# Optimization experiments

Measured on AMD Instinct MI355X. Metric: run time of the kernel, lower is better.

## Reference

```python
import math
import jax, jax.numpy as jnp
import numpy as np

H = 12  # n_heads
NEG = -1e9

def setup_inputs() -> dict:
    key = jax.random.key(0)
    ks = jax.random.split(key, 5)
    B, S, D = 1, 4096, 768
    x = jax.random.normal(ks[0], (B, S, D), dtype=jnp.float32)
    Wqkv = jax.random.normal(ks[1], (D, 3 * D), dtype=jnp.float32) * (1.0 / math.sqrt(D))
    bqkv = jnp.zeros((3 * D,), dtype=jnp.float32)
    Wout = jax.random.normal(ks[2], (D, D), dtype=jnp.float32) * (1.0 / math.sqrt(D))
    bout = jnp.zeros((D,), dtype=jnp.float32)
    rel_bias = jax.random.normal(ks[3], (H, S, S), dtype=jnp.float32) * 0.02
    # additive causal mask: 0 on/below diagonal, large negative above
    causal_mask = jnp.where(jnp.tril(jnp.ones((S, S), dtype=bool)), 0.0, NEG).astype(jnp.float32)
    return {"x": x, "Wqkv": Wqkv, "bqkv": bqkv, "Wout": Wout, "bout": bout,
            "rel_bias": rel_bias, "causal_mask": causal_mask}

def reference(x, Wqkv, bqkv, Wout, bout, rel_bias, causal_mask):
    B, S, D = x.shape
    hd = D // H
    qkv = x @ Wqkv + bqkv                      # [B,S,3D]
    q, k, v = jnp.split(qkv, 3, axis=-1)
    def heads(t):  # [B,S,D] -> [B,H,S,hd]
        return t.reshape(B, S, H, hd).transpose(0, 2, 1, 3)
    q, k, v = heads(q), heads(k), heads(v)
    scores = jnp.einsum('bhqd,bhkd->bhqk', q, k) / math.sqrt(hd)
    scores = scores + rel_bias[None] + causal_mask[None, None]
    attn = jax.nn.softmax(scores, axis=-1)     # dropout p=0.0 -> identity
    out = jnp.einsum('bhqk,bhkd->bhqd', attn, v)
    out = out.transpose(0, 2, 1, 3).reshape(B, S, D)
    return out @ Wout + bout
```

## Files before the change

### kernel.cpp

```cpp
#include <hip/hip_runtime.h>
#include <stdint.h>

typedef _Float16 f16;
typedef _Float16 f16x8 __attribute__((ext_vector_type(8)));
typedef _Float16 f16x4 __attribute__((ext_vector_type(4)));
typedef float f32x4 __attribute__((ext_vector_type(4)));

#define NEGF -1e30f

static __device__ __forceinline__ f32x4 mfma16(f16x8 a, f16x8 b, f32x4 c) {
    return __builtin_amdgcn_mfma_f32_16x16x32_f16(a, b, c, 0, 0, 0);
}

static __device__ __forceinline__ void gload_lds16(const void* g, void* l) {
    __builtin_amdgcn_global_load_lds(
        (const __attribute__((address_space(1))) unsigned int*)g,
        (__attribute__((address_space(3))) unsigned int*)l, 16, 0, 0);
}

__global__ void cast_f32_f16(const float* __restrict__ src, f16* __restrict__ dst, int n) {
    int idx = blockIdx.x * blockDim.x + threadIdx.x;
    int stride = gridDim.x * blockDim.x;
    for (int i = idx * 4; i < n; i += stride * 4) {
        float4 v = *(const float4*)(src + i);
        f16x4 h;
        h[0] = (f16)v.x; h[1] = (f16)v.y; h[2] = (f16)v.z; h[3] = (f16)v.w;
        *(f16x4*)(dst + i) = h;
    }
}

__global__ void transpose_cast(const float* __restrict__ src, f16* __restrict__ dst, int R, int C) {
    __shared__ float tile[32][33];
    const int c0 = blockIdx.x * 32, r0 = blockIdx.y * 32;
    const int tx = threadIdx.x & 31, ty = threadIdx.x >> 5;
#pragma unroll
    for (int i = 0; i < 32; i += 8)
        tile[ty + i][tx] = src[(size_t)(r0 + ty + i) * C + c0 + tx];
    __syncthreads();
#pragma unroll
    for (int i = 0; i < 32; i += 8)
        dst[(size_t)(c0 + ty + i) * R + r0 + tx] = (f16)tile[tx][ty + i];
}

template <int MODE>
__global__ void __launch_bounds__(256, 2)
gemm_f16(const f16* __restrict__ A, const f16* __restrict__ Bt,
         const float* __restrict__ bias,
         f16* __restrict__ Qb, f16* __restrict__ Kb, f16* __restrict__ Vtb,
         float* __restrict__ Cout, int K, int N) {
    __shared__ alignas(16) f16 As[128 * 32];
    __shared__ alignas(16) f16 Bs[128 * 32];
    const int t = threadIdx.x;
    const int lane = t & 63, wid = t >> 6;
    const int wm = wid >> 1, wn = wid & 1;
    const int lr = lane & 15, lg = lane >> 4;
    const int m0 = blockIdx.y * 128, n0 = blockIdx.x * 128;
    f32x4 acc[4][4] = {};
    for (int k0 = 0; k0 < K; k0 += 32) {
#pragma unroll
        for (int i = 0; i < 2; i++) {
            const int cc = t + i * 256;
            const int rr = cc >> 2, ch = cc & 3;
            gload_lds16(A + (size_t)(m0 + rr) * K + k0 + ch * 8, (f16*)As + cc * 8);
            gload_lds16(Bt + (size_t)(n0 + rr) * K + k0 + ch * 8, (f16*)Bs + cc * 8);
        }
        __syncthreads();
        f16x8 af[4], bf[4];
#pragma unroll
        for (int i = 0; i < 4; i++)
            af[i] = *(const f16x8*)(As + (wm * 64 + i * 16 + lr) * 32 + lg * 8);
#pragma unroll
        for (int j = 0; j < 4; j++)
            bf[j] = *(const f16x8*)(Bs + (wn * 64 + j * 16 + lr) * 32 + lg * 8);
#pragma unroll
        for (int i = 0; i < 4; i++)
#pragma unroll
            for (int j = 0; j < 4; j++)
                acc[i][j] = mfma16(af[i], bf[j], acc[i][j]);
        __syncthreads();
    }
#pragma unroll
    for (int i = 0; i < 4; i++) {
#pragma unroll
        for (int j = 0; j < 4; j++) {
            const int n_g = n0 + wn * 64 + j * 16 + lr;
            const float bv = bias[n_g];
#pragma unroll
            for (int jj = 0; jj < 4; jj++) {
                const int m_g = m0 + wm * 64 + i * 16 + lg * 4 + jj;
                const float val = acc[i][j][jj] + bv;
                if (MODE == 0) {
                    if (n_g < 768) {
                        Qb[(((n_g >> 6) * 4096) + m_g) * 64 + (n_g & 63)] = (f16)(val * 0.125f);
                    } else if (n_g < 1536) {
                        const int n2 = n_g - 768;
                        Kb[(((n2 >> 6) * 4096) + m_g) * 64 + (n2 & 63)] = (f16)val;
                    } else {
                        const int n2 = n_g - 1536;
                        Vtb[((n2 >> 6) * 64 + (n2 & 63)) * 4096 + m_g] = (f16)val;
                    }
                } else {
                    Cout[(size_t)m_g * N + n_g] = val;
                }
            }
        }
    }
}

__global__ void __launch_bounds__(256, 2)
attn_fwd(const f16* __restrict__ Qb, const f16* __restrict__ Kb,
         const f16* __restrict__ Vtb, const float* __restrict__ rel_bias,
         f16* __restrict__ Opart, float* __restrict__ mpart, float* __restrict__ lpart) {
    __shared__ alignas(16) f16 Ks[64 * 64];
    __shared__ alignas(16) f16 Vs[64 * 64];
    __shared__ alignas(16) f16 Ps[4][64 * 72];
    __shared__ alignas(16) float fac[4][64];
    const int bid = blockIdx.x;
    const int h = bid / 72;
    int rr = bid % 72;
    int Q = 0;
    for (;;) { const int n = (Q + 2) >> 1; if (rr < n) break; rr -= n; ++Q; }
    const int c = rr;
    const int lo = c * 8;
    const int hi = min(lo + 8, 4 * Q + 4);

    const int t = threadIdx.x, lane = t & 63, wid = t >> 6;
    const int lr = lane & 15, lg = lane >> 4;
    const int g = 4 * Q + wid;
    const int q0w = g * 64;
    const f16* Qh = Qb + (size_t)h * 4096 * 64;
    const f16* Kh = Kb + (size_t)h * 4096 * 64;
    const f16* Vh = Vtb + (size_t)h * 64 * 4096;
    const float* rbh = rel_bias + (size_t)h * 4096 * 4096;

    f16x8 qf[4][2];
#pragma unroll
    for (int nf = 0; nf < 4; nf++)
#pragma unroll
        for (int kd = 0; kd < 2; kd++)
            qf[nf][kd] = *(const f16x8*)(Qh + (size_t)(q0w + nf * 16 + lr) * 64 + kd * 32 + lg * 8);

    f32x4 o[4][4] = {};
    float mrow[4] = {NEGF, NEGF, NEGF, NEGF};
    float lrow[4] = {0.f, 0.f, 0.f, 0.f};
    const int qmaxw = q0w + 63;

    for (int kt = lo; kt < hi; kt++) {
        const int kbase = kt * 64;
#pragma unroll
        for (int i = 0; i < 2; i++) {
            const int cc = t + i * 256;
            const int row = cc >> 3;
            const int cswz = (((cc & 7) * 16) ^ ((row & 7) << 4)) >> 1;
            gload_lds16(Kh + (size_t)(kbase + row) * 64 + cswz, (f16*)Ks + cc * 8);
            gload_lds16(Vh + (size_t)row * 4096 + kbase + cswz, (f16*)Vs + cc * 8);
        }
        __syncthreads();
        if (kbase <= qmaxw) {
            f32x4 st[4][4] = {};
#pragma unroll
            for (int kd = 0; kd < 2; kd++) {
#pragma unroll
                for (int mf = 0; mf < 4; mf++) {
                    const int r = mf * 16 + lr;
                    const int cf = ((kd * 64 + lg * 16) ^ ((r & 7) << 4)) >> 1;
                    const f16x8 kf = *(const f16x8*)(Ks + r * 64 + cf);
#pragma unroll
                    for (int nf = 0; nf < 4; nf++)
                        st[mf][nf] = mfma16(kf, qf[nf][kd], st[mf][nf]);
                }
            }
#pragma unroll
            for (int nf = 0; nf < 4; nf++) {
                const int q_g = q0w + nf * 16 + lr;
                const float* rbrow = rbh + (size_t)q_g * 4096 + kbase;
                float mx = NEGF;
#pragma unroll
                for (int mf = 0; mf < 4; mf++) {
                    const float4 rb = *(const float4*)(rbrow + mf * 16 + lg * 4);
                    const float rbv[4] = {rb.x, rb.y, rb.z, rb.w};
#pragma unroll
                    for (int jj = 0; jj < 4; jj++) {
                        const int k_g = kbase + mf * 16 + lg * 4 + jj;
                        float v = st[mf][nf][jj] + rbv[jj];
                        v = (k_g > q_g) ? NEGF : v;
                        st[mf][nf][jj] = v;
                        mx = fmaxf(mx, v);
                    }
                }
                mx = fmaxf(mx, __shfl_xor(mx, 16));
                mx = fmaxf(mx, __shfl_xor(mx, 32));
                const float mnew = fmaxf(mrow[nf], mx);
                const float fscale = __expf(mrow[nf] - mnew);
                mrow[nf] = mnew;
                float rsum = 0.f;
#pragma unroll
                for (int mf = 0; mf < 4; mf++) {
                    f16x4 pv;
#pragma unroll
                    for (int jj = 0; jj < 4; jj++) {
                        const float p = __expf(st[mf][nf][jj] - mnew);
                        rsum += p;
                        pv[jj] = (f16)p;
                    }
                    *(f16x4*)(&Ps[wid][(nf * 16 + lr) * 72 + mf * 16 + lg * 4]) = pv;
                }
                rsum += __shfl_xor(rsum, 16);
                rsum += __shfl_xor(rsum, 32);
                lrow[nf] = lrow[nf] * fscale + rsum;
                if (lane < 16) fac[wid][nf * 16 + lr] = fscale;
            }
            asm volatile("s_waitcnt lgkmcnt(0)" ::: "memory");
#pragma unroll
            for (int mf2 = 0; mf2 < 4; mf2++) {
                const float4 fv = *(const float4*)&fac[wid][mf2 * 16 + lg * 4];
                const float fvv[4] = {fv.x, fv.y, fv.z, fv.w};
#pragma unroll
                for (int nf2 = 0; nf2 < 4; nf2++)
#pragma unroll
                    for (int jj = 0; jj < 4; jj++)
                        o[mf2][nf2][jj] *= fvv[jj];
            }
#pragma unroll
            for (int kk = 0; kk < 2; kk++) {
                f16x8 pa[4], vb[4];
#pragma unroll
                for (int mf2 = 0; mf2 < 4; mf2++)
                    pa[mf2] = *(const f16x8*)(&Ps[wid][(mf2 * 16 + lr) * 72 + kk * 32 + lg * 8]);
#pragma unroll
                for (int nf2 = 0; nf2 < 4; nf2++) {
                    const int r = nf2 * 16 + lr;
                    const int cf = ((kk * 64 + lg * 16) ^ ((r & 7) << 4)) >> 1;
                    vb[nf2] = *(const f16x8*)(Vs + r * 64 + cf);
                }
#pragma unroll
                for (int mf2 = 0; mf2 < 4; mf2++)
#pragma unroll
                    for (int nf2 = 0; nf2 < 4; nf2++)
                        o[mf2][nf2] = mfma16(pa[mf2], vb[nf2], o[mf2][nf2]);
            }
        }
        __syncthreads();
    }

    const int s = (h * 64 + g) * 8 + c;
    f16* Op = Opart + (size_t)s * 4096;
#pragma unroll
    for (int mf2 = 0; mf2 < 4; mf2++)
#pragma unroll
        for (int nf2 = 0; nf2 < 4; nf2++)
#pragma unroll
            for (int jj = 0; jj < 4; jj++)
                Op[(mf2 * 16 + lg * 4 + jj) * 64 + nf2 * 16 + lr] = (f16)o[mf2][nf2][jj];
    if (lg == 0) {
#pragma unroll
        for (int nf = 0; nf < 4; nf++) {
            mpart[(size_t)s * 64 + nf * 16 + lr] = mrow[nf];
            lpart[(size_t)s * 64 + nf * 16 + lr] = lrow[nf];
        }
    }
}

__global__ void __launch_bounds__(256)
merge_norm(const f16* __restrict__ Opart, const float* __restrict__ mpart,
           const float* __restrict__ lpart, f16* __restrict__ Ob) {
    const int g = blockIdx.x, h = blockIdx.y;
    const int nc = ((g >> 2) + 2) >> 1;
    const int t = threadIdx.x;
    const int row = t >> 2, cq = t & 3;
    const size_t base = (size_t)((h * 64 + g) * 8);
    float M = NEGF;
#pragma unroll
    for (int i = 0; i < 8; i++)
        if (i < nc) M = fmaxf(M, mpart[(base + i) * 64 + row]);
    float L = 0.f;
    float acc0[8] = {}, acc1[8] = {};
#pragma unroll
    for (int i = 0; i < 8; i++) {
        if (i < nc) {
            const float w = __expf(mpart[(base + i) * 64 + row] - M);
            L += w * lpart[(base + i) * 64 + row];
            const f16x8 a = *(const f16x8*)(Opart + (base + i) * 4096 + row * 64 + cq * 16);
            const f16x8 b = *(const f16x8*)(Opart + (base + i) * 4096 + row * 64 + cq * 16 + 8);
#pragma unroll
            for (int j = 0; j < 8; j++) {
                acc0[j] += w * (float)a[j];
                acc1[j] += w * (float)b[j];
            }
        }
    }
    const float inv = 1.f / L;
    const int q = g * 64 + row;
    f16x8 o0, o1;
#pragma unroll
    for (int j = 0; j < 8; j++) { o0[j] = (f16)(acc0[j] * inv); o1[j] = (f16)(acc1[j] * inv); }
    *(f16x8*)(Ob + (size_t)q * 768 + h * 64 + cq * 16) = o0;
    *(f16x8*)(Ob + (size_t)q * 768 + h * 64 + cq * 16 + 8) = o1;
}

extern "C" void kernel_launch(void* const* d_in, const int* in_sizes, int n_in,
                              void* d_out, int out_size, void* d_ws, size_t ws_size,
                              hipStream_t stream) {
    const float* x = (const float*)d_in[0];
    const float* Wqkv = (const float*)d_in[1];
    const float* bqkv = (const float*)d_in[2];
    const float* Wout = (const float*)d_in[3];
    const float* bout = (const float*)d_in[4];
    const float* rel_bias = (const float*)d_in[5];
    float* out = (float*)d_out;

    f16* p = (f16*)d_ws;
    f16* xb = p;     p += (size_t)4096 * 768;
    f16* WqkvT = p;  p += (size_t)2304 * 768;
    f16* WoutT = p;  p += (size_t)768 * 768;
    f16* Qb = p;     p += (size_t)12 * 4096 * 64;
    f16* Kb = p;     p += (size_t)12 * 4096 * 64;
    f16* Vtb = p;    p += (size_t)12 * 4096 * 64;
    f16* Ob = p;     p += (size_t)4096 * 768;
    f16* Opart = p;  p += (size_t)6144 * 4096;
    float* fp = (float*)p;
    float* mpart = fp;  fp += (size_t)6144 * 64;
    float* lpart = fp;  fp += (size_t)6144 * 64;

    cast_f32_f16<<<3072, 256, 0, stream>>>(x, xb, 4096 * 768);
    transpose_cast<<<dim3(2304 / 32, 768 / 32), 256, 0, stream>>>(Wqkv, WqkvT, 768, 2304);
    transpose_cast<<<dim3(768 / 32, 768 / 32), 256, 0, stream>>>(Wout, WoutT, 768, 768);
    gemm_f16<0><<<dim3(18, 32), 256, 0, stream>>>(xb, WqkvT, bqkv, Qb, Kb, Vtb, nullptr, 768, 2304);
    attn_fwd<<<dim3(864), 256, 0, stream>>>(Qb, Kb, Vtb, rel_bias, Opart, mpart, lpart);
    merge_norm<<<dim3(64, 12), 256, 0, stream>>>(Opart, mpart, lpart, Ob);
    gemm_f16<1><<<dim3(6, 32), 256, 0, stream>>>(Ob, WoutT, bout, nullptr, nullptr, nullptr, out, 768, 768);
}
```

Before: 227.1 us.

## Shrink attention per-wave query tile to 32 rows and double grid

```diff
diff --git a/kernel.cpp b/kernel.cpp
--- a/kernel.cpp
+++ b/kernel.cpp
@@ -107,43 +107,43 @@
     }
 }
 
-__global__ void __launch_bounds__(256, 2)
+__global__ void __launch_bounds__(256, 3)
 attn_fwd(const f16* __restrict__ Qb, const f16* __restrict__ Kb,
          const f16* __restrict__ Vtb, const float* __restrict__ rel_bias,
          f16* __restrict__ Opart, float* __restrict__ mpart, float* __restrict__ lpart) {
     __shared__ alignas(16) f16 Ks[64 * 64];
     __shared__ alignas(16) f16 Vs[64 * 64];
-    __shared__ alignas(16) f16 Ps[4][64 * 72];
-    __shared__ alignas(16) float fac[4][64];
+    __shared__ alignas(16) f16 Ps[4][32 * 72];
+    __shared__ alignas(16) float fac[4][32];
     const int bid = blockIdx.x;
-    const int h = bid / 72;
-    int rr = bid % 72;
-    int Q = 0;
-    for (;;) { const int n = (Q + 2) >> 1; if (rr < n) break; rr -= n; ++Q; }
+    const int h = bid / 144;
+    int rr = bid % 144;
+    int qb = 0;
+    for (;;) { const int n = (qb + 4) >> 2; if (rr < n) break; rr -= n; ++qb; }
     const int c = rr;
     const int lo = c * 8;
-    const int hi = min(lo + 8, 4 * Q + 4);
+    const int hi = min(lo + 8, 2 * qb + 2);
 
     const int t = threadIdx.x, lane = t & 63, wid = t >> 6;
     const int lr = lane & 15, lg = lane >> 4;
-    const int g = 4 * Q + wid;
-    const int q0w = g * 64;
+    const int g = qb * 4 + wid;
+    const int q0w = g * 32;
+    const int ktd = g >> 1;
     const f16* Qh = Qb + (size_t)h * 4096 * 64;
     const f16* Kh = Kb + (size_t)h * 4096 * 64;
     const f16* Vh = Vtb + (size_t)h * 64 * 4096;
     const float* rbh = rel_bias + (size_t)h * 4096 * 4096;
 
-    f16x8 qf[4][2];
-#pragma unroll
-    for (int nf = 0; nf < 4; nf++)
+    f16x8 qf[2][2];
+#pragma unroll
+    for (int nf = 0; nf < 2; nf++)
 #pragma unroll
         for (int kd = 0; kd < 2; kd++)
             qf[nf][kd] = *(const f16x8*)(Qh + (size_t)(q0w + nf * 16 + lr) * 64 + kd * 32 + lg * 8);
 
-    f32x4 o[4][4] = {};
-    float mrow[4] = {NEGF, NEGF, NEGF, NEGF};
-    float lrow[4] = {0.f, 0.f, 0.f, 0.f};
-    const int qmaxw = q0w + 63;
+    f32x4 o[2][4] = {};
+    float mrow[2] = {NEGF, NEGF};
+    float lrow[2] = {0.f, 0.f};
 
     for (int kt = lo; kt < hi; kt++) {
         const int kbase = kt * 64;
@@ -156,8 +156,14 @@
             gload_lds16(Vh + (size_t)row * 4096 + kbase + cswz, (f16*)Vs + cc * 8);
         }
         __syncthreads();
-        if (kbase <= qmaxw) {
-            f32x4 st[4][4] = {};
+        if (kt <= ktd) {
+            float4 rb[2][4];
+#pragma unroll
+            for (int nf = 0; nf < 2; nf++)
+#pragma unroll
+                for (int mf = 0; mf < 4; mf++)
+                    rb[nf][mf] = *(const float4*)(rbh + (size_t)(q0w + nf * 16 + lr) * 4096 + kbase + mf * 16 + lg * 4);
+            f32x4 st[4][2] = {};
 #pragma unroll
             for (int kd = 0; kd < 2; kd++) {
 #pragma unroll
@@ -166,24 +172,25 @@
                     const int cf = ((kd * 64 + lg * 16) ^ ((r & 7) << 4)) >> 1;
                     const f16x8 kf = *(const f16x8*)(Ks + r * 64 + cf);
 #pragma unroll
-                    for (int nf = 0; nf < 4; nf++)
+                    for (int nf = 0; nf < 2; nf++)
                         st[mf][nf] = mfma16(kf, qf[nf][kd], st[mf][nf]);
                 }
             }
-#pragma unroll
-            for (int nf = 0; nf < 4; nf++) {
+            const bool diag = (kt == ktd);
+#pragma unroll
+            for (int nf = 0; nf < 2; nf++) {
                 const int q_g = q0w + nf * 16 + lr;
-                const float* rbrow = rbh + (size_t)q_g * 4096 + kbase;
                 float mx = NEGF;
 #pragma unroll
                 for (int mf = 0; mf < 4; mf++) {
-                    const float4 rb = *(const float4*)(rbrow + mf * 16 + lg * 4);
-                    const float rbv[4] = {rb.x, rb.y, rb.z, rb.w};
+                    const float rbv[4] = {rb[nf][mf].x, rb[nf][mf].y, rb[nf][mf].z, rb[nf][mf].w};
 #pragma unroll
                     for (int jj = 0; jj < 4; jj++) {
-                        const int k_g = kbase + mf * 16 + lg * 4 + jj;
                         float v = st[mf][nf][jj] + rbv[jj];
-                        v = (k_g > q_g) ? NEGF : v;
+                        if (diag) {
+                            const int k_g = kbase + mf * 16 + lg * 4 + jj;
+                            v = (k_g > q_g) ? NEGF : v;
+                        }
                         st[mf][nf][jj] = v;
                         mx = fmaxf(mx, v);
                     }
@@ -212,51 +219,51 @@
             }
             asm volatile("s_waitcnt lgkmcnt(0)" ::: "memory");
 #pragma unroll
-            for (int mf2 = 0; mf2 < 4; mf2++) {
-                const float4 fv = *(const float4*)&fac[wid][mf2 * 16 + lg * 4];
+            for (int qf2 = 0; qf2 < 2; qf2++) {
+                const float4 fv = *(const float4*)&fac[wid][qf2 * 16 + lg * 4];
                 const float fvv[4] = {fv.x, fv.y, fv.z, fv.w};
 #pragma unroll
-                for (int nf2 = 0; nf2 < 4; nf2++)
+                for (int df = 0; df < 4; df++)
 #pragma unroll
                     for (int jj = 0; jj < 4; jj++)
-                        o[mf2][nf2][jj] *= fvv[jj];
+                        o[qf2][df][jj] *= fvv[jj];
             }
 #pragma unroll
             for (int kk = 0; kk < 2; kk++) {
-                f16x8 pa[4], vb[4];
-#pragma unroll
-                for (int mf2 = 0; mf2 < 4; mf2++)
-                    pa[mf2] = *(const f16x8*)(&Ps[wid][(mf2 * 16 + lr) * 72 + kk * 32 + lg * 8]);
-#pragma unroll
-                for (int nf2 = 0; nf2 < 4; nf2++) {
-                    const int r = nf2 * 16 + lr;
+                f16x8 pa[2], vb[4];
+#pragma unroll
+                for (int qf2 = 0; qf2 < 2; qf2++)
+                    pa[qf2] = *(const f16x8*)(&Ps[wid][(qf2 * 16 + lr) * 72 + kk * 32 + lg * 8]);
+#pragma unroll
+                for (int df = 0; df < 4; df++) {
+                    const int r = df * 16 + lr;
                     const int cf = ((kk * 64 + lg * 16) ^ ((r & 7) << 4)) >> 1;
-                    vb[nf2] = *(const f16x8*)(Vs + r * 64 + cf);
-                }
-#pragma unroll
-                for (int mf2 = 0; mf2 < 4; mf2++)
-#pragma unroll
-                    for (int nf2 = 0; nf2 < 4; nf2++)
-                        o[mf2][nf2] = mfma16(pa[mf2], vb[nf2], o[mf2][nf2]);
+                    vb[df] = *(const f16x8*)(Vs + r * 64 + cf);
+                }
+#pragma unroll
+                for (int qf2 = 0; qf2 < 2; qf2++)
+#pragma unroll
+                    for (int df = 0; df < 4; df++)
+                        o[qf2][df] = mfma16(pa[qf2], vb[df], o[qf2][df]);
             }
         }
         __syncthreads();
     }
 
-    const int s = (h * 64 + g) * 8 + c;
-    f16* Op = Opart + (size_t)s * 4096;
-#pragma unroll
-    for (int mf2 = 0; mf2 < 4; mf2++)
-#pragma unroll
-        for (int nf2 = 0; nf2 < 4; nf2++)
+    const int s = (h * 128 + g) * 8 + c;
+    f16* Op = Opart + (size_t)s * 2048;
+#pragma unroll
+    for (int qf2 = 0; qf2 < 2; qf2++)
+#pragma unroll
+        for (int df = 0; df < 4; df++)
 #pragma unroll
             for (int jj = 0; jj < 4; jj++)
-                Op[(mf2 * 16 + lg * 4 + jj) * 64 + nf2 * 16 + lr] = (f16)o[mf2][nf2][jj];
+                Op[(qf2 * 16 + lg * 4 + jj) * 64 + df * 16 + lr] = (f16)o[qf2][df][jj];
     if (lg == 0) {
 #pragma unroll
-        for (int nf = 0; nf < 4; nf++) {
-            mpart[(size_t)s * 64 + nf * 16 + lr] = mrow[nf];
-            lpart[(size_t)s * 64 + nf * 16 + lr] = lrow[nf];
+        for (int nf = 0; nf < 2; nf++) {
+            mpart[(size_t)s * 32 + nf * 16 + lr] = mrow[nf];
+            lpart[(size_t)s * 32 + nf * 16 + lr] = lrow[nf];
         }
     }
 }
@@ -264,38 +271,45 @@
 __global__ void __launch_bounds__(256)
 merge_norm(const f16* __restrict__ Opart, const float* __restrict__ mpart,
            const float* __restrict__ lpart, f16* __restrict__ Ob) {
+    __shared__ float wls[8][32];
+    __shared__ float Linv[32];
     const int g = blockIdx.x, h = blockIdx.y;
-    const int nc = ((g >> 2) + 2) >> 1;
+    const int nc = (g >> 4) + 1;
+    const size_t sb = (size_t)(h * 128 + g) * 8;
     const int t = threadIdx.x;
-    const int row = t >> 2, cq = t & 3;
-    const size_t base = (size_t)((h * 64 + g) * 8);
-    float M = NEGF;
-#pragma unroll
-    for (int i = 0; i < 8; i++)
-        if (i < nc) M = fmaxf(M, mpart[(base + i) * 64 + row]);
-    float L = 0.f;
-    float acc0[8] = {}, acc1[8] = {};
+    if (t < 32) {
+        float M = NEGF;
+#pragma unroll
+        for (int i = 0; i < 8; i++)
+            if (i < nc) M = fmaxf(M, mpart[(sb + i) * 32 + t]);
+        float L = 0.f;
+#pragma unroll
+        for (int i = 0; i < 8; i++)
+            if (i < nc) {
+                const float w = __expf(mpart[(sb + i) * 32 + t] - M);
+                wls[i][t] = w;
+                L += w * lpart[(sb + i) * 32 + t];
+            }
+        Linv[t] = 1.f / L;
+    }
+    __syncthreads();
+    const int row = t >> 3, dq = t & 7;
+    float acc[8] = {};
 #pragma unroll
     for (int i = 0; i < 8; i++) {
         if (i < nc) {
-            const float w = __expf(mpart[(base + i) * 64 + row] - M);
-            L += w * lpart[(base + i) * 64 + row];
-            const f16x8 a = *(const f16x8*)(Opart + (base + i) * 4096 + row * 64 + cq * 16);
-            const f16x8 b = *(const f16x8*)(Opart + (base + i) * 4096 + row * 64 + cq * 16 + 8);
-#pragma unroll
-            for (int j = 0; j < 8; j++) {
-                acc0[j] += w * (float)a[j];
-                acc1[j] += w * (float)b[j];
-            }
-        }
-    }
-    const float inv = 1.f / L;
-    const int q = g * 64 + row;
-    f16x8 o0, o1;
-#pragma unroll
-    for (int j = 0; j < 8; j++) { o0[j] = (f16)(acc0[j] * inv); o1[j] = (f16)(acc1[j] * inv); }
-    *(f16x8*)(Ob + (size_t)q * 768 + h * 64 + cq * 16) = o0;
-    *(f16x8*)(Ob + (size_t)q * 768 + h * 64 + cq * 16 + 8) = o1;
+            const f16x8 a = *(const f16x8*)(Opart + (sb + i) * 2048 + row * 64 + dq * 8);
+            const float w = wls[i][row];
+#pragma unroll
+            for (int j = 0; j < 8; j++) acc[j] += w * (float)a[j];
+        }
+    }
+    const float inv = Linv[row];
+    const int q = g * 32 + row;
+    f16x8 ov;
+#pragma unroll
+    for (int j = 0; j < 8; j++) ov[j] = (f16)(acc[j] * inv);
+    *(f16x8*)(Ob + (size_t)q * 768 + h * 64 + dq * 8) = ov;
 }
 
 extern "C" void kernel_launch(void* const* d_in, const int* in_sizes, int n_in,
@@ -317,16 +331,16 @@
     f16* Kb = p;     p += (size_t)12 * 4096 * 64;
     f16* Vtb = p;    p += (size_t)12 * 4096 * 64;
     f16* Ob = p;     p += (size_t)4096 * 768;
-    f16* Opart = p;  p += (size_t)6144 * 4096;
+    f16* Opart = p;  p += (size_t)12 * 128 * 8 * 2048;
     float* fp = (float*)p;
-    float* mpart = fp;  fp += (size_t)6144 * 64;
-    float* lpart = fp;  fp += (size_t)6144 * 64;
+    float* mpart = fp;  fp += (size_t)12 * 128 * 8 * 32;
+    float* lpart = fp;  fp += (size_t)12 * 128 * 8 * 32;
 
     cast_f32_f16<<<3072, 256, 0, stream>>>(x, xb, 4096 * 768);
     transpose_cast<<<dim3(2304 / 32, 768 / 32), 256, 0, stream>>>(Wqkv, WqkvT, 768, 2304);
     transpose_cast<<<dim3(768 / 32, 768 / 32), 256, 0, stream>>>(Wout, WoutT, 768, 768);
     gemm_f16<0><<<dim3(18, 32), 256, 0, stream>>>(xb, WqkvT, bqkv, Qb, Kb, Vtb, nullptr, 768, 2304);
-    attn_fwd<<<dim3(864), 256, 0, stream>>>(Qb, Kb, Vtb, rel_bias, Opart, mpart, lpart);
-    merge_norm<<<dim3(64, 12), 256, 0, stream>>>(Opart, mpart, lpart, Ob);
+    attn_fwd<<<dim3(1728), 256, 0, stream>>>(Qb, Kb, Vtb, rel_bias, Opart, mpart, lpart);
+    merge_norm<<<dim3(128, 12), 256, 0, stream>>>(Opart, mpart, lpart, Ob);
     gemm_f16<1><<<dim3(6, 32), 256, 0, stream>>>(Ob, WoutT, bout, nullptr, nullptr, nullptr, out, 768, 768);
 }
```

Result: no change. 225.1 us (-0.9%).
